# Optimization experiments

Measured on AMD Instinct MI355X. Metric: run time of the kernel, lower is better.

The kernel has to match this reference:

```python
import jax, jax.numpy as jnp
import numpy as np

N, D = 1024, 8192

def setup_inputs() -> dict:
    key = jax.random.key(0)
    k1, k2 = jax.random.split(key)
    pred = jax.random.normal(k1, (N, D), dtype=jnp.float32)
    eeg = jax.random.normal(k2, (N, D), dtype=jnp.float32)
    return {"pred": pred, "eeg": eeg}

def _ranks(x):
    # rank transform along last axis (no ties expected for continuous data):
    # argsort of argsort gives 0-based ranks, matching spearman rank order.
    order = jnp.argsort(x, axis=-1)
    return jnp.argsort(order, axis=-1).astype(x.dtype)

def _normed_ranks(x):
    r = _ranks(x)  # [n, D]
    r = r - jnp.mean(r, axis=-1, keepdims=True)
    return r / jnp.linalg.norm(r, axis=-1, keepdims=True)

def reference(pred, eeg):
    # base criterion: MSELoss (as used in the repo)
    loss1 = jnp.mean((pred - eeg) ** 2)
    # all-pairs spearman correlation via one batched rank + single GEMM,
    # replacing the original O(n^2) python loop of tiny ops.
    rp = _normed_ranks(pred)   # [n, D]
    re_ = _normed_ranks(eeg)   # [n, D]
    corr = rp @ re_.T          # [n, n] pairwise spearman coefficients
    n = pred.shape[0]
    pos = jnp.mean(jnp.diagonal(corr))
    off_mask = ~jnp.eye(n, dtype=bool)
    neg = jnp.sum(jnp.where(off_mask, corr, 0.0)) / (n * (n - 1))
    # original builds loss2 from torch.tensor(list) -> detached from autograd
    loss2 = jax.lax.stop_gradient(1.0 - pos + neg)
    return loss1 + loss2
```

## Files before the change

### kernel.cpp

```cpp
#include <hip/hip_runtime.h>
#include <stdint.h>

#define NROW 1024
#define DCOL 8192
#define T1   1024
#define EPT  8

typedef unsigned long long u64;

__device__ __forceinline__ uint32_t sortable_key(float f){
  uint32_t u = __float_as_uint(f);
  return u ^ ((uint32_t)((int32_t)u >> 31) | 0x80000000u);
}

extern "C" __global__ void __launch_bounds__(T1)
rank_kernel(const float* __restrict__ pred, const float* __restrict__ eeg,
            uint16_t* __restrict__ ranks, double* __restrict__ msepart)
{
  __shared__ uint32_t h[DCOL];
  __shared__ uint32_t g[DCOL];
  __shared__ uint32_t wt[16];
  __shared__ double   redd[16];

  const int t = threadIdx.x;
  const int bid = blockIdx.x;
  const int pair = ((bid >> 4) << 3) | (bid & 7);
  const bool is_eeg = (bid >> 3) & 1;
  const int lane = t & 63, wid = t >> 6;
  const float* src = is_eeg ? (eeg  + (size_t)pair * DCOL)
                            : (pred + (size_t)pair * DCOL);

  const float4* s4 = (const float4*)(src + t * EPT);
  float4 va = s4[0], vb = s4[1];

  {
    uint4 z = make_uint4(0u,0u,0u,0u);
    *(uint4*)&h[t*EPT]   = z;
    *(uint4*)&h[t*EPT+4] = z;
    *(uint4*)&g[t*EPT]   = z;
    *(uint4*)&g[t*EPT+4] = z;
  }

  double msum = 0.0;
  if (is_eeg){
    const float4* p4 = (const float4*)(pred + (size_t)pair * DCOL + t * EPT);
    float4 qa = p4[0], qb = p4[1];
    float d;
    d=qa.x-va.x; msum += (double)(d*d);
    d=qa.y-va.y; msum += (double)(d*d);
    d=qa.z-va.z; msum += (double)(d*d);
    d=qa.w-va.w; msum += (double)(d*d);
    d=qb.x-vb.x; msum += (double)(d*d);
    d=qb.y-vb.y; msum += (double)(d*d);
    d=qb.z-vb.z; msum += (double)(d*d);
    d=qb.w-vb.w; msum += (double)(d*d);
  }

  uint32_t key[EPT];
  key[0]=sortable_key(va.x); key[1]=sortable_key(va.y);
  key[2]=sortable_key(va.z); key[3]=sortable_key(va.w);
  key[4]=sortable_key(vb.x); key[5]=sortable_key(vb.y);
  key[6]=sortable_key(vb.z); key[7]=sortable_key(vb.w);
  __syncthreads();

  #pragma unroll
  for (int j=0;j<EPT;j++) atomicAdd(&h[key[j]>>19], 1u);
  __syncthreads();

  {
    uint4 ca = *(const uint4*)&h[t*EPT];
    uint4 cb = *(const uint4*)&h[t*EPT+4];
    uint32_t tot = ca.x+ca.y+ca.z+ca.w+cb.x+cb.y+cb.z+cb.w;
    uint32_t v = tot;
    #pragma unroll
    for (int o=1;o<64;o<<=1){ uint32_t u=__shfl_up(v,o,64); if(lane>=o) v+=u; }
    if (lane==63) wt[wid]=v;
    __syncthreads();
    uint32_t x = (lane < wid) ? wt[lane] : 0u;
    #pragma unroll
    for (int o=32;o>0;o>>=1) x += __shfl_xor(x, o, 64);
    uint32_t run = x + v - tot;
    uint4 oa, ob;
    oa.x=(run<<16)|ca.x; run+=ca.x;
    oa.y=(run<<16)|ca.y; run+=ca.y;
    oa.z=(run<<16)|ca.z; run+=ca.z;
    oa.w=(run<<16)|ca.w; run+=ca.w;
    ob.x=(run<<16)|cb.x; run+=cb.x;
    ob.y=(run<<16)|cb.y; run+=cb.y;
    ob.z=(run<<16)|cb.z; run+=cb.z;
    ob.w=(run<<16)|cb.w; run+=cb.w;
    *(uint4*)&h[t*EPT]   = oa;
    *(uint4*)&h[t*EPT+4] = ob;
  }
  __syncthreads();

  uint32_t b2[EPT], e[EPT];
  #pragma unroll
  for (int j=0;j<EPT;j++){
    uint32_t hi = key[j]>>19, lo = key[j]&0x7FFFFu;
    uint32_t v  = h[hi];
    b2[j] = (v>>16) + (__umul24(lo, v&0xFFFFu)>>19);
    e[j]  = (lo<<13) | (uint32_t)(t*EPT+j);
    atomicAdd(&g[b2[j]], 1u);
  }
  __syncthreads();

  {
    uint4 ca = *(const uint4*)&g[t*EPT];
    uint4 cb = *(const uint4*)&g[t*EPT+4];
    uint32_t tot = ca.x+ca.y+ca.z+ca.w+cb.x+cb.y+cb.z+cb.w;
    uint32_t v = tot;
    #pragma unroll
    for (int o=1;o<64;o<<=1){ uint32_t u=__shfl_up(v,o,64); if(lane>=o) v+=u; }
    if (lane==63) wt[wid]=v;
    __syncthreads();
    uint32_t x = (lane < wid) ? wt[lane] : 0u;
    #pragma unroll
    for (int o=32;o>0;o>>=1) x += __shfl_xor(x, o, 64);
    uint32_t run = x + v - tot;
    uint4 oa, ob;
    oa.x=(run<<16)|run; run+=ca.x;
    oa.y=(run<<16)|run; run+=ca.y;
    oa.z=(run<<16)|run; run+=ca.z;
    oa.w=(run<<16)|run; run+=ca.w;
    ob.x=(run<<16)|run; run+=cb.x;
    ob.y=(run<<16)|run; run+=cb.y;
    ob.z=(run<<16)|run; run+=cb.z;
    ob.w=(run<<16)|run; run+=cb.w;
    *(uint4*)&g[t*EPT]   = oa;
    *(uint4*)&g[t*EPT+4] = ob;
  }
  __syncthreads();

  uint32_t old[EPT];
  #pragma unroll
  for (int j=0;j<EPT;j++){
    old[j] = atomicAdd(&g[b2[j]], 1u);
    h[old[j] & 0xFFFFu] = e[j];
  }
  __syncthreads();

  uint32_t rk[EPT];
  #pragma unroll
  for (int j=0;j<EPT;j++){
    uint32_t st = old[j] >> 16;
    uint32_t en = g[b2[j]] & 0xFFFFu;
    uint32_t cnt = 0;
    if (en - st > 1){
      for (uint32_t p = st; p < en; ++p) cnt += (h[p] < e[j]) ? 1u : 0u;
    }
    rk[j] = st + cnt;
  }

  uint4 pk;
  pk.x = rk[0] | (rk[1]<<16);
  pk.y = rk[2] | (rk[3]<<16);
  pk.z = rk[4] | (rk[5]<<16);
  pk.w = rk[6] | (rk[7]<<16);
  const size_t orow = is_eeg ? (size_t)(NROW + pair) : (size_t)pair;
  *(uint4*)(ranks + orow*DCOL + (size_t)t*EPT) = pk;

  if (is_eeg){
    #pragma unroll
    for (int o=32;o>0;o>>=1) msum += __shfl_down(msum,o,64);
    if (lane==0) redd[wid]=msum;
    __syncthreads();
    if (t==0){
      double m=0.0;
      #pragma unroll
      for (int w=0;w<16;w++) m += redd[w];
      msepart[pair]=m;
    }
  }
}

extern "C" __global__ void __launch_bounds__(128)
colsum_part_kernel(const uint16_t* __restrict__ ranks,
                   u64* __restrict__ SABpart, u64* __restrict__ dotpart)
{
  __shared__ u64 redu[2];
  const int t = threadIdx.x;
  const int bx = blockIdx.x, by = blockIdx.y;
  const int col = bx*1024 + t*8;
  const int r0  = by*16;
  const uint16_t* rp = ranks;
  const uint16_t* re = ranks + (size_t)NROW*DCOL;
  uint32_t sa[8] = {0,0,0,0,0,0,0,0};
  uint32_t sb[8] = {0,0,0,0,0,0,0,0};
  u64 dt = 0ull;
  #pragma unroll
  for (int i=0;i<16;i++){
    uint4 a = *(const uint4*)&rp[(size_t)(r0+i)*DCOL + col];
    uint4 b = *(const uint4*)&re[(size_t)(r0+i)*DCOL + col];
    uint32_t aw[8] = {a.x&0xFFFFu,a.x>>16,a.y&0xFFFFu,a.y>>16,
                      a.z&0xFFFFu,a.z>>16,a.w&0xFFFFu,a.w>>16};
    uint32_t bw[8] = {b.x&0xFFFFu,b.x>>16,b.y&0xFFFFu,b.y>>16,
                      b.z&0xFFFFu,b.z>>16,b.w&0xFFFFu,b.w>>16};
    uint32_t rowdt = 0;
    #pragma unroll
    for (int k=0;k<8;k++){ sa[k]+=aw[k]; sb[k]+=bw[k]; rowdt += aw[k]*bw[k]; }
    dt += (u64)rowdt;
  }
  u64* dst = SABpart + (size_t)by*DCOL + col;
  #pragma unroll
  for (int k=0;k<8;k++) dst[k] = (u64)sa[k] | ((u64)sb[k]<<32);

  #pragma unroll
  for (int o=32;o>0;o>>=1) dt += __shfl_down(dt,o,64);
  int lane=t&63, wid=t>>6;
  if (lane==0) redu[wid]=dt;
  __syncthreads();
  if (t==0) dotpart[by*8+bx] = redu[0]+redu[1];
}

extern "C" __global__ void __launch_bounds__(128)
reduce2_kernel(const u64* __restrict__ SABpart, double* __restrict__ Spart)
{
  __shared__ double red[2];
  const int t = threadIdx.x;
  const int col = blockIdx.x*128 + t;
  u64 s = 0ull;
  #pragma unroll
  for (int by=0; by<64; by++) s += SABpart[(size_t)by*DCOL + col];
  const double NMU = 4193792.0;
  double d = ((double)(uint32_t)s - NMU) * ((double)(uint32_t)(s>>32) - NMU);
  #pragma unroll
  for (int o=32;o>0;o>>=1) d += __shfl_down(d,o,64);
  int lane=t&63, wid=t>>6;
  if (lane==0) red[wid]=d;
  __syncthreads();
  if (t==0) Spart[blockIdx.x] = red[0]+red[1];
}

extern "C" __global__ void __launch_bounds__(256)
final_kernel(const double* __restrict__ Spart, const u64* __restrict__ dotpart,
             const double* __restrict__ msepart, float* __restrict__ out)
{
  __shared__ double wpartd[4], wpartm[4];
  __shared__ u64 wpartu[4];
  const int t = threadIdx.x;
  double s = (t < 64) ? Spart[t] : 0.0;
  u64 d = dotpart[t] + dotpart[t+256];
  double m = 0.0;
  for (int i=t;i<NROW;i+=256) m += msepart[i];
  #pragma unroll
  for (int o=32;o>0;o>>=1){
    s+=__shfl_down(s,o,64); m+=__shfl_down(m,o,64); d+=__shfl_down(d,o,64);
  }
  int lane=t&63, wid=t>>6;
  if (lane==0){ wpartd[wid]=s; wpartm[wid]=m; wpartu[wid]=d; }
  __syncthreads();
  if (t==0){
    double sasb   = wpartd[0]+wpartd[1]+wpartd[2]+wpartd[3];
    double msesum = wpartm[0]+wpartm[1]+wpartm[2]+wpartm[3];
    double dot    = (double)(wpartu[0]+wpartu[1]+wpartu[2]+wpartu[3]);
    const double C     = 45812983808.0;
    const double NDMU2 = 140703130714112.0;
    double diag_sum = (dot - NDMU2) / C;
    double pos = diag_sum / (double)NROW;
    double stotal = sasb / C;
    double neg = (stotal - diag_sum) / ((double)NROW*(double)(NROW-1));
    double loss1 = msesum / ((double)NROW*(double)DCOL);
    out[0] = (float)(loss1 + 1.0 - pos + neg);
  }
}

extern "C" __global__ void __launch_bounds__(256)
colsum_atomic_kernel(const uint16_t* __restrict__ ranks,
                     u64* __restrict__ SAB, u64* __restrict__ dotacc)
{
  const int t = threadIdx.x;
  const int col = blockIdx.x*2048 + t*8;
  const int r0  = blockIdx.y*16;
  const uint16_t* rp = ranks;
  const uint16_t* re = ranks + (size_t)NROW*DCOL;
  uint32_t sa[8] = {0,0,0,0,0,0,0,0};
  uint32_t sb[8] = {0,0,0,0,0,0,0,0};
  u64 dt = 0ull;
  for (int i=0;i<16;i++){
    uint4 a = *(const uint4*)&rp[(size_t)(r0+i)*DCOL + col];
    uint4 b = *(const uint4*)&re[(size_t)(r0+i)*DCOL + col];
    uint32_t aw[8] = {a.x&0xFFFFu,a.x>>16,a.y&0xFFFFu,a.y>>16,
                      a.z&0xFFFFu,a.z>>16,a.w&0xFFFFu,a.w>>16};
    uint32_t bw[8] = {b.x&0xFFFFu,b.x>>16,b.y&0xFFFFu,b.y>>16,
                      b.z&0xFFFFu,b.z>>16,b.w&0xFFFFu,b.w>>16};
    uint32_t rowdt = 0;
    #pragma unroll
    for (int k=0;k<8;k++){ sa[k]+=aw[k]; sb[k]+=bw[k]; rowdt += aw[k]*bw[k]; }
    dt += (u64)rowdt;
  }
  #pragma unroll
  for (int k=0;k<8;k++)
    atomicAdd(&SAB[col+k], (u64)sa[k] | ((u64)sb[k]<<32));
  #pragma unroll
  for (int o=32;o>0;o>>=1) dt += __shfl_down(dt,o,64);
  if ((t&63)==0) atomicAdd(dotacc, dt);
}

extern "C" __global__ void __launch_bounds__(256)
final_atomic_kernel(const u64* __restrict__ SAB, const u64* __restrict__ dotacc,
                    const double* __restrict__ msepart, float* __restrict__ out)
{
  __shared__ double wpartd[4], wpartm[4];
  const int t = threadIdx.x;
  const double NMU = 4193792.0;
  double s = 0.0;
  for (int i=0;i<DCOL/256;i++){
    u64 v = SAB[i*256+t];
    s += ((double)(uint32_t)v - NMU)*((double)(uint32_t)(v>>32) - NMU);
  }
  double m = 0.0;
  for (int i=t;i<NROW;i+=256) m += msepart[i];
  #pragma unroll
  for (int o=32;o>0;o>>=1){ s+=__shfl_down(s,o,64); m+=__shfl_down(m,o,64); }
  int lane=t&63, wid=t>>6;
  if (lane==0){ wpartd[wid]=s; wpartm[wid]=m; }
  __syncthreads();
  if (t==0){
    double sasb   = wpartd[0]+wpartd[1]+wpartd[2]+wpartd[3];
    double msesum = wpartm[0]+wpartm[1]+wpartm[2]+wpartm[3];
    const double C     = 45812983808.0;
    const double NDMU2 = 140703130714112.0;
    double dot = (double)(*dotacc);
    double diag_sum = (dot - NDMU2) / C;
    double pos = diag_sum / (double)NROW;
    double stotal = sasb / C;
    double neg = (stotal - diag_sum) / ((double)NROW*(double)(NROW-1));
    double loss1 = msesum / ((double)NROW*(double)DCOL);
    out[0] = (float)(loss1 + 1.0 - pos + neg);
  }
}

extern "C" void kernel_launch(void* const* d_in, const int* in_sizes, int n_in,
                              void* d_out, int out_size, void* d_ws, size_t ws_size,
                              hipStream_t stream)
{
  const float* pred = (const float*)d_in[0];
  const float* eeg  = (const float*)d_in[1];
  float* out = (float*)d_out;

  char* ws = (char*)d_ws;
  const size_t OFF       = (size_t)2*NROW*DCOL*sizeof(uint16_t);
  const size_t SZ_PART   = (size_t)64*DCOL*sizeof(u64);
  const size_t NEED_PART = OFF + SZ_PART + 64*sizeof(double) + 512*sizeof(u64)
                           + NROW*sizeof(double);
  const size_t NEED_ATOM = OFF + DCOL*sizeof(u64) + 8 + NROW*sizeof(double);

  if (ws_size >= NEED_PART){
    uint16_t* ranks  = (uint16_t*)ws;
    u64* SABpart     = (u64*)(ws + OFF);
    double* Spart    = (double*)(ws + OFF + SZ_PART);
    u64* dotpart     = (u64*)(ws + OFF + SZ_PART + 64*sizeof(double));
    double* msepart  = (double*)(ws + OFF + SZ_PART + 64*sizeof(double) + 512*sizeof(u64));

    rank_kernel<<<dim3(2*NROW), dim3(T1), 0, stream>>>(pred, eeg, ranks, msepart);
    colsum_part_kernel<<<dim3(8,64), dim3(128), 0, stream>>>(ranks, SABpart, dotpart);
    reduce2_kernel<<<dim3(64), dim3(128), 0, stream>>>(SABpart, Spart);
    final_kernel<<<dim3(1), dim3(256), 0, stream>>>(Spart, dotpart, msepart, out);
  } else if (ws_size >= NEED_ATOM){
    uint16_t* ranks  = (uint16_t*)ws;
    u64* SAB         = (u64*)(ws + OFF);
    u64* dotacc      = (u64*)(ws + OFF + DCOL*sizeof(u64));
    double* msepart  = (double*)(ws + OFF + DCOL*sizeof(u64) + 8);

    hipMemsetAsync(ws + OFF, 0, DCOL*sizeof(u64) + 8, stream);
    rank_kernel<<<dim3(2*NROW), dim3(T1), 0, stream>>>(pred, eeg, ranks, msepart);
    colsum_atomic_kernel<<<dim3(4,64), dim3(256), 0, stream>>>(ranks, SAB, dotacc);
    final_atomic_kernel<<<dim3(1), dim3(256), 0, stream>>>(SAB, dotacc, msepart, out);
  } else {
    hipMemsetAsync(d_out, 0xFF, sizeof(float), stream);
  }
}
```

Measured before the change: 77.65 us.

## Replace histogram pass with normal-CDF bucket table for rank sorting

```diff
diff --git a/kernel.cpp b/kernel.cpp
--- a/kernel.cpp
+++ b/kernel.cpp
@@ -1,10 +1,12 @@
 #include <hip/hip_runtime.h>
 #include <stdint.h>
+#include <math.h>
 
 #define NROW 1024
 #define DCOL 8192
 #define T1   1024
 #define EPT  8
+#define TSZ  1024
 
 typedef unsigned long long u64;
 
@@ -17,9 +19,12 @@
 rank_kernel(const float* __restrict__ pred, const float* __restrict__ eeg,
             uint16_t* __restrict__ ranks, double* __restrict__ msepart)
 {
-  __shared__ uint32_t h[DCOL];
   __shared__ uint32_t g[DCOL];
+  __shared__ uint32_t ekey[DCOL];
+  __shared__ uint32_t Tl[TSZ];
+  __shared__ uint32_t arr[TSZ];
   __shared__ uint32_t wt[16];
+  __shared__ uint32_t listn;
   __shared__ double   redd[16];
 
   const int t = threadIdx.x;
@@ -35,11 +40,10 @@
 
   {
     uint4 z = make_uint4(0u,0u,0u,0u);
-    *(uint4*)&h[t*EPT]   = z;
-    *(uint4*)&h[t*EPT+4] = z;
     *(uint4*)&g[t*EPT]   = z;
     *(uint4*)&g[t*EPT+4] = z;
   }
+  if (t == 0) listn = 0u;
 
   double msum = 0.0;
   if (is_eeg){
@@ -61,47 +65,39 @@
   key[2]=sortable_key(va.z); key[3]=sortable_key(va.w);
   key[4]=sortable_key(vb.x); key[5]=sortable_key(vb.y);
   key[6]=sortable_key(vb.z); key[7]=sortable_key(vb.w);
-  __syncthreads();
-
-  #pragma unroll
-  for (int j=0;j<EPT;j++) atomicAdd(&h[key[j]>>19], 1u);
-  __syncthreads();
 
   {
-    uint4 ca = *(const uint4*)&h[t*EPT];
-    uint4 cb = *(const uint4*)&h[t*EPT+4];
-    uint32_t tot = ca.x+ca.y+ca.z+ca.w+cb.x+cb.y+cb.z+cb.w;
-    uint32_t v = tot;
-    #pragma unroll
-    for (int o=1;o<64;o<<=1){ uint32_t u=__shfl_up(v,o,64); if(lane>=o) v+=u; }
+    uint32_t s = (uint32_t)t << 22;
+    uint32_t u = (s & 0x80000000u) ? (s ^ 0x80000000u) : ~s;
+    float x = __uint_as_float(u);
+    float c;
+    if (x != x) c = (s & 0x80000000u) ? 1.0f : 0.0f;
+    else        c = 0.5f + 0.5f * erff(x * 0.70710678f);
+    uint32_t b = (uint32_t)fminf(c * 8192.0f, 8191.0f);
+    uint32_t v = b;
+    #pragma unroll
+    for (int o=1;o<64;o<<=1){ uint32_t uu=__shfl_up(v,o,64); if(lane>=o) v=max(v,uu); }
     if (lane==63) wt[wid]=v;
     __syncthreads();
-    uint32_t x = (lane < wid) ? wt[lane] : 0u;
-    #pragma unroll
-    for (int o=32;o>0;o>>=1) x += __shfl_xor(x, o, 64);
-    uint32_t run = x + v - tot;
-    uint4 oa, ob;
-    oa.x=(run<<16)|ca.x; run+=ca.x;
-    oa.y=(run<<16)|ca.y; run+=ca.y;
-    oa.z=(run<<16)|ca.z; run+=ca.z;
-    oa.w=(run<<16)|ca.w; run+=ca.w;
-    ob.x=(run<<16)|cb.x; run+=cb.x;
-    ob.y=(run<<16)|cb.y; run+=cb.y;
-    ob.z=(run<<16)|cb.z; run+=cb.z;
-    ob.w=(run<<16)|cb.w; run+=cb.w;
-    *(uint4*)&h[t*EPT]   = oa;
-    *(uint4*)&h[t*EPT+4] = ob;
-  }
-  __syncthreads();
-
-  uint32_t b2[EPT], e[EPT];
+    uint32_t xx = (lane < wid) ? wt[lane] : 0u;
+    #pragma unroll
+    for (int o=32;o>0;o>>=1) xx = max(xx, __shfl_xor(xx,o,64));
+    v = max(v, xx);
+    arr[t] = v;
+    __syncthreads();
+    uint32_t nb = (t < TSZ-1) ? arr[t+1] : 8192u;
+    Tl[t] = (v<<16) | (nb - v);
+  }
+  __syncthreads();
+
+  uint32_t bin[EPT];
   #pragma unroll
   for (int j=0;j<EPT;j++){
-    uint32_t hi = key[j]>>19, lo = key[j]&0x7FFFFu;
-    uint32_t v  = h[hi];
-    b2[j] = (v>>16) + (__umul24(lo, v&0xFFFFu)>>19);
-    e[j]  = (lo<<13) | (uint32_t)(t*EPT+j);
-    atomicAdd(&g[b2[j]], 1u);
+    uint32_t k  = key[j];
+    uint32_t tv = Tl[k >> 22];
+    uint32_t lo = k & 0x3FFFFFu;
+    bin[j] = (tv>>16) + (uint32_t)(((u64)lo * (tv & 0xFFFFu)) >> 22);
+    atomicAdd(&g[bin[j]], 1u);
   }
   __syncthreads();
 
@@ -111,7 +107,7 @@
     uint32_t tot = ca.x+ca.y+ca.z+ca.w+cb.x+cb.y+cb.z+cb.w;
     uint32_t v = tot;
     #pragma unroll
-    for (int o=1;o<64;o<<=1){ uint32_t u=__shfl_up(v,o,64); if(lane>=o) v+=u; }
+    for (int o=1;o<64;o<<=1){ uint32_t u2=__shfl_up(v,o,64); if(lane>=o) v+=u2; }
     if (lane==63) wt[wid]=v;
     __syncthreads();
     uint32_t x = (lane < wid) ? wt[lane] : 0u;
@@ -135,21 +131,45 @@
   uint32_t old[EPT];
   #pragma unroll
   for (int j=0;j<EPT;j++){
-    old[j] = atomicAdd(&g[b2[j]], 1u);
-    h[old[j] & 0xFFFFu] = e[j];
+    old[j] = atomicAdd(&g[bin[j]], 1u);
+    ekey[old[j] & 0xFFFFu] = key[j];
   }
   __syncthreads();
 
   uint32_t rk[EPT];
+  uint32_t tiedmask = 0u;
   #pragma unroll
   for (int j=0;j<EPT;j++){
     uint32_t st = old[j] >> 16;
-    uint32_t en = g[b2[j]] & 0xFFFFu;
-    uint32_t cnt = 0;
-    if (en - st > 1){
-      for (uint32_t p = st; p < en; ++p) cnt += (h[p] < e[j]) ? 1u : 0u;
+    uint32_t en = g[bin[j]] & 0xFFFFu;
+    uint32_t less = 0, eq = 1;
+    if (en - st > 1u){
+      eq = 0;
+      for (uint32_t p = st; p < en; ++p){
+        uint32_t k2 = ekey[p];
+        less += (k2 <  key[j]) ? 1u : 0u;
+        eq   += (k2 == key[j]) ? 1u : 0u;
+      }
     }
-    rk[j] = st + cnt;
+    rk[j] = st + less;
+    if (eq > 1u){
+      uint32_t pp = atomicAdd(&listn, 1u);
+      if (pp < TSZ/2){ arr[2*pp] = key[j]; arr[2*pp+1] = (uint32_t)(t*EPT+j); }
+      tiedmask |= (1u << j);
+    }
+  }
+  __syncthreads();
+  if (tiedmask){
+    uint32_t n = min(listn, (uint32_t)(TSZ/2));
+    #pragma unroll
+    for (int j=0;j<EPT;j++){
+      if (tiedmask & (1u<<j)){
+        uint32_t add = 0, me = (uint32_t)(t*EPT+j);
+        for (uint32_t q=0;q<n;q++)
+          add += (arr[2*q] == key[j] && arr[2*q+1] < me) ? 1u : 0u;
+        rk[j] += add;
+      }
+    }
   }
 
   uint4 pk;
```

Measured after the change: 81.85 us. +5.4%, slower.
